# Optimization experiments

Measured on AMD Instinct MI355X. Metric: run time of the kernel, lower is better.

Reference implementation:

```python
import jax, jax.numpy as jnp
import numpy as np

B, T, D, H, FF = 4, 2048, 1024, 16, 4096
HD = D // H
EPS = 1e-5


def setup_inputs() -> dict:
    key = jax.random.key(0)
    ks = jax.random.split(key, 10)
    s = lambda k, shape, fan: jax.random.normal(k, shape, jnp.float32) * (1.0 / np.sqrt(fan))
    return {
        "x": jax.random.normal(ks[0], (B, T, D), jnp.float32),
        "ln1_g": jnp.ones((D,), jnp.float32),
        "ln1_b": jnp.zeros((D,), jnp.float32),
        "qkv_w": s(ks[1], (D, 3 * D), D),
        "qkv_b": jnp.zeros((3 * D,), jnp.float32),
        "proj_w": s(ks[2], (D, D), D),
        "proj_b": jnp.zeros((D,), jnp.float32),
        "ln2_g": jnp.ones((D,), jnp.float32),
        "ln2_b": jnp.zeros((D,), jnp.float32),
        "ff1_w": s(ks[3], (D, FF), D),
        "ff1_b": jnp.zeros((FF,), jnp.float32),
        "ff2_w": s(ks[4], (FF, D), FF),
        "ff2_b": jnp.zeros((D,), jnp.float32),
    }


def _layernorm(x, g, b):
    mu = jnp.mean(x, axis=-1, keepdims=True)
    var = jnp.mean(jnp.square(x - mu), axis=-1, keepdims=True)
    return (x - mu) * jax.lax.rsqrt(var + EPS) * g + b


def reference(x, ln1_g, ln1_b, qkv_w, qkv_b, proj_w, proj_b,
              ln2_g, ln2_b, ff1_w, ff1_b, ff2_w, ff2_b):
    # --- attention sublayer ---
    h = _layernorm(x, ln1_g, ln1_b)
    qkv = h @ qkv_w + qkv_b                      # [B,T,3D]
    q, k, v = jnp.split(qkv, 3, axis=-1)
    q = q.reshape(B, T, H, HD).transpose(0, 2, 1, 3)  # [B,H,T,hd]
    k = k.reshape(B, T, H, HD).transpose(0, 2, 1, 3)
    v = v.reshape(B, T, H, HD).transpose(0, 2, 1, 3)
    att = jnp.einsum('bhqd,bhkd->bhqk', q, k) / np.sqrt(HD)
    causal = jnp.tril(jnp.ones((T, T), bool))
    att = jnp.where(causal, att, jnp.finfo(att.dtype).min)
    att = jax.nn.softmax(att, axis=-1)
    out = jnp.einsum('bhqk,bhkd->bhqd', att, v)  # [B,H,T,hd]
    out = out.transpose(0, 2, 1, 3).reshape(B, T, D)
    x = x + out @ proj_w + proj_b
    # --- MLP sublayer ---
    h = _layernorm(x, ln2_g, ln2_b)
    h = jax.nn.gelu(h @ ff1_w + ff1_b, approximate=True)
    x = x + h @ ff2_w + ff2_b
    return x
```

## Files before the change

### kernel.cpp

```cpp
#include <hip/hip_runtime.h>

typedef __attribute__((ext_vector_type(4))) float f32x4;
typedef __attribute__((ext_vector_type(8))) short s16x8;
typedef __attribute__((ext_vector_type(4))) unsigned short u16x4;

#define DEV __device__ __forceinline__

DEV unsigned short f2bf(float f) {
  unsigned int u = __float_as_uint(f);
  return (unsigned short)((u + 0x7FFFu + ((u >> 16) & 1u)) >> 16);
}

DEV void gload_lds16(const void* g, void* l) {
  __builtin_amdgcn_global_load_lds(
      (const __attribute__((address_space(1))) unsigned int*)g,
      (__attribute__((address_space(3))) unsigned int*)l, 16, 0, 0);
}

__global__ __launch_bounds__(256) void ln_kernel(
    const float* __restrict__ x, const float* __restrict__ gam,
    const float* __restrict__ bet, unsigned short* __restrict__ o)
{
  const int row = blockIdx.x;
  const int tid = threadIdx.x;
  f32x4 v = *(const f32x4*)(x + (size_t)row * 1024 + tid * 4);
  float s = v[0] + v[1] + v[2] + v[3];
  float s2 = v[0]*v[0] + v[1]*v[1] + v[2]*v[2] + v[3]*v[3];
  #pragma unroll
  for (int m = 1; m < 64; m <<= 1) { s += __shfl_xor(s, m); s2 += __shfl_xor(s2, m); }
  __shared__ float ps[4], ps2[4];
  const int wid = tid >> 6, lane = tid & 63;
  if (lane == 0) { ps[wid] = s; ps2[wid] = s2; }
  __syncthreads();
  s = ps[0] + ps[1] + ps[2] + ps[3];
  s2 = ps2[0] + ps2[1] + ps2[2] + ps2[3];
  const float mu = s * (1.0f / 1024.0f);
  const float rstd = rsqrtf(s2 * (1.0f / 1024.0f) - mu * mu + 1e-5f);
  f32x4 g4 = *(const f32x4*)(gam + tid * 4);
  f32x4 b4 = *(const f32x4*)(bet + tid * 4);
  u16x4 ov;
  #pragma unroll
  for (int j = 0; j < 4; j++) ov[j] = f2bf((v[j] - mu) * rstd * g4[j] + b4[j]);
  *(u16x4*)(o + (size_t)row * 1024 + tid * 4) = ov;
}

__global__ __launch_bounds__(256) void transpose_kernel(
    const float* __restrict__ W, unsigned short* __restrict__ WT, int K, int N)
{
  __shared__ float tile[64][65];
  const int n0 = blockIdx.x * 64, k0 = blockIdx.y * 64;
  const int c = threadIdx.x & 63, r0 = threadIdx.x >> 6;
  #pragma unroll
  for (int r = r0; r < 64; r += 4)
    tile[r][c] = W[(size_t)(k0 + r) * N + n0 + c];
  __syncthreads();
  #pragma unroll
  for (int r = r0; r < 64; r += 4)
    WT[(size_t)(n0 + r) * K + k0 + c] = f2bf(tile[c][r]);
}

template <int MODE>
__global__ __launch_bounds__(256) void gemm_kernel(
    const unsigned short* __restrict__ A, const unsigned short* __restrict__ WT,
    const float* __restrict__ bias, const float* resid, void* outp,
    int M, int N, int K)
{
  __shared__ unsigned short As[128 * 32];
  __shared__ unsigned short Bs[128 * 32];
  const int tid = threadIdx.x;
  const int lane = tid & 63;
  const int wid = tid >> 6;
  const int l15 = lane & 15, l4 = lane >> 4;
  const int tiles_n = N >> 7;
  const int cpx = gridDim.x >> 3;
  const int id = (blockIdx.x & 7) * cpx + (blockIdx.x >> 3);
  const int bm = id / tiles_n, bn = id % tiles_n;
  const int wr = wid >> 1, wc = wid & 1;

  f32x4 acc[4][4] = {};

  for (int kt = 0; kt < K; kt += 32) {
    #pragma unroll
    for (int s = 0; s < 2; ++s) {
      const int c = s * 256 + tid;
      const int rowi = c >> 2, colb = (c & 3) * 8;
      unsigned short* lbase_a = As + (size_t)(c & ~63) * 8;
      unsigned short* lbase_b = Bs + (size_t)(c & ~63) * 8;
      gload_lds16(A  + (size_t)(bm * 128 + rowi) * K + kt + colb, lbase_a);
      gload_lds16(WT + (size_t)(bn * 128 + rowi) * K + kt + colb, lbase_b);
    }
    __syncthreads();
    s16x8 af[4], bq[4];
    #pragma unroll
    for (int i = 0; i < 4; i++)
      af[i] = *(const s16x8*)&As[(wr * 64 + i * 16 + l15) * 32 + l4 * 8];
    #pragma unroll
    for (int j = 0; j < 4; j++)
      bq[j] = *(const s16x8*)&Bs[(wc * 64 + j * 16 + l15) * 32 + l4 * 8];
    #pragma unroll
    for (int i = 0; i < 4; i++)
      #pragma unroll
      for (int j = 0; j < 4; j++)
        acc[i][j] = __builtin_amdgcn_mfma_f32_16x16x32_bf16(af[i], bq[j], acc[i][j], 0, 0, 0);
    __syncthreads();
  }

  #pragma unroll
  for (int i = 0; i < 4; i++) {
    #pragma unroll
    for (int j = 0; j < 4; j++) {
      const int col = bn * 128 + wc * 64 + j * 16 + l15;
      const float bv = bias[col];
      #pragma unroll
      for (int r = 0; r < 4; r++) {
        const int row = bm * 128 + wr * 64 + i * 16 + l4 * 4 + r;
        const size_t off = (size_t)row * N + col;
        float v = acc[i][j][r] + bv;
        if (MODE == 1) {
          ((float*)outp)[off] = v + resid[off];
        } else if (MODE == 2) {
          const float t = __expf(1.5957691216f * (v + 0.044715f * v * v * v));
          ((unsigned short*)outp)[off] = f2bf(v - v / (t + 1.0f));
        } else {
          ((unsigned short*)outp)[off] = f2bf(v);
        }
      }
    }
  }
}


struct AttnState {
  f32x4 o[4];
  float m, l;
};

DEV void attn_tile(const s16x8* qf, const unsigned short* Ks,
                   const unsigned short* Vt, unsigned short* Pw,
                   AttnState& st, int kv0, int qg, int l15, int l4, bool need_mask)
{
  f32x4 sa[4];
  #pragma unroll
  for (int cb = 0; cb < 4; cb++) sa[cb] = (f32x4){0.f, 0.f, 0.f, 0.f};
  __builtin_amdgcn_s_setprio(1);
  #pragma unroll
  for (int ks = 0; ks < 2; ++ks) {
    #pragma unroll
    for (int cb = 0; cb < 4; cb++) {
      const int kvr = cb * 16 + l15;
      s16x8 bk = *(const s16x8*)&Ks[kvr * 64 + ((ks * 32 + l4 * 8) ^ ((kvr & 7) << 3))];
      sa[cb] = __builtin_amdgcn_mfma_f32_16x16x32_bf16(bk, qf[ks], sa[cb], 0, 0, 0);
    }
  }
  __builtin_amdgcn_s_setprio(0);
  float mx = -3.0e38f;
  const int thr = qg - kv0 - l4 * 4;
  #pragma unroll
  for (int cb = 0; cb < 4; cb++)
    #pragma unroll
    for (int r = 0; r < 4; r++) {
      float sv = sa[cb][r] * 0.125f;
      if (need_mask && (cb * 16 + r > thr)) sv = -3.0e38f;
      sa[cb][r] = sv;
      mx = fmaxf(mx, sv);
    }
  mx = fmaxf(mx, __shfl_xor(mx, 16));
  mx = fmaxf(mx, __shfl_xor(mx, 32));
  const float mnew = fmaxf(st.m, mx);
  const float alpha = __expf(st.m - mnew);
  st.m = mnew;
  float rsum = 0.f;
  #pragma unroll
  for (int cb = 0; cb < 4; cb++) {
    u16x4 pw;
    #pragma unroll
    for (int r = 0; r < 4; r++) {
      const float p = __expf(sa[cb][r] - mnew);
      rsum += p;
      pw[r] = f2bf(p);
    }
    *(u16x4*)&Pw[l15 * 64 + ((cb * 16 + l4 * 4) ^ ((l15 & 7) << 3))] = pw;
  }
  rsum += __shfl_xor(rsum, 16);
  rsum += __shfl_xor(rsum, 32);
  st.l = st.l * alpha + rsum;
  #pragma unroll
  for (int r = 0; r < 4; r++) {
    const float ar = __shfl(alpha, l4 * 4 + r);
    #pragma unroll
    for (int cb = 0; cb < 4; cb++) st.o[cb][r] *= ar;
  }
  asm volatile("s_waitcnt lgkmcnt(0)" ::: "memory");
  __builtin_amdgcn_s_setprio(1);
  #pragma unroll
  for (int ks = 0; ks < 2; ++ks) {
    s16x8 pa = *(const s16x8*)&Pw[l15 * 64 + ((ks * 32 + l4 * 8) ^ ((l15 & 7) << 3))];
    #pragma unroll
    for (int cb = 0; cb < 4; cb++) {
      const int d = cb * 16 + l15;
      s16x8 vf = *(const s16x8*)&Vt[d * 64 + ((ks * 32 + l4 * 8) ^ (((d >> 2) & 7) << 3))];
      st.o[cb] = __builtin_amdgcn_mfma_f32_16x16x32_bf16(pa, vf, st.o[cb], 0, 0, 0);
    }
  }
  __builtin_amdgcn_s_setprio(0);
}

DEV void attn_write(unsigned short* orow, const AttnState& st, int l15, int l4) {
  const float invl = 1.0f / st.l;
  #pragma unroll
  for (int r = 0; r < 4; r++) {
    const float ir = __shfl(invl, l4 * 4 + r);
    #pragma unroll
    for (int cb = 0; cb < 4; cb++)
      orow[(l4 * 4 + r) * 1024 + cb * 16 + l15] = f2bf(st.o[cb][r] * ir);
  }
}

__global__ __launch_bounds__(256) void attn_kernel(
    const unsigned short* __restrict__ qkv, unsigned short* __restrict__ outb)
{
  __shared__ unsigned short Ks[64 * 64];
  __shared__ unsigned short Vt[64 * 64];
  __shared__ unsigned short Ps[2][4][16 * 64];
  const int pid = blockIdx.x;
  const int qA = pid, qB = 31 - pid;
  const int bh = blockIdx.y;
  const int b = bh >> 4, h = bh & 15;
  const int tid = threadIdx.x, lane = tid & 63, wid = tid >> 6;
  const int l15 = lane & 15, l4 = lane >> 4;
  const size_t base = (size_t)b * 2048 * 3072 + (size_t)h * 64;
  const unsigned short* Qb = qkv + base;
  const unsigned short* Kb = qkv + base + 1024;
  const unsigned short* Vb = qkv + base + 2048;

  s16x8 qfA[2], qfB[2];
  {
    const unsigned short* qr = Qb + (size_t)(qA * 64 + wid * 16 + l15) * 3072 + l4 * 8;
    qfA[0] = *(const s16x8*)qr;
    qfA[1] = *(const s16x8*)(qr + 32);
    qr = Qb + (size_t)(qB * 64 + wid * 16 + l15) * 3072 + l4 * 8;
    qfB[0] = *(const s16x8*)qr;
    qfB[1] = *(const s16x8*)(qr + 32);
  }
  AttnState sA, sB;
  #pragma unroll
  for (int cb = 0; cb < 4; cb++) {
    sA.o[cb] = (f32x4){0.f, 0.f, 0.f, 0.f};
    sB.o[cb] = (f32x4){0.f, 0.f, 0.f, 0.f};
  }
  sA.m = -1e30f; sA.l = 0.f; sB.m = -1e30f; sB.l = 0.f;
  const int qgA = qA * 64 + wid * 16 + l15;
  const int qgB = qB * 64 + wid * 16 + l15;

  for (int kvb = 0; kvb <= qB; ++kvb) {
    const int kv0 = kvb * 64;
    __syncthreads();
    #pragma unroll
    for (int s = 0; s < 2; ++s) {
      const int c = s * 256 + tid;
      const int kv = c >> 3;
      const int dsrc = ((c & 7) * 8) ^ ((kv & 7) << 3);
      gload_lds16(Kb + (size_t)(kv0 + kv) * 3072 + dsrc,
                  Ks + (size_t)(c & ~63) * 8);
    }
    #pragma unroll
    for (int it = 0; it < 4; ++it) {
      const int cc = tid + 256 * it;
      const int vkv = cc >> 4;
      const int vd = (cc & 15) * 4;
      u16x4 vv = *(const u16x4*)(Vb + (size_t)(kv0 + vkv) * 3072 + vd);
      #pragma unroll
      for (int j = 0; j < 4; j++) {
        const int d = vd + j;
        Vt[d * 64 + (vkv ^ (((d >> 2) & 7) << 3))] = vv[j];
      }
    }
    __syncthreads();

    if (kvb <= qA)
      attn_tile(qfA, Ks, Vt, Ps[0][wid], sA, kv0, qgA, l15, l4,
                kv0 + 63 > qA * 64 + wid * 16);
    attn_tile(qfB, Ks, Vt, Ps[1][wid], sB, kv0, qgB, l15, l4,
              kv0 + 63 > qB * 64 + wid * 16);
  }
  attn_write(outb + ((size_t)b * 2048 + qA * 64 + wid * 16) * 1024 + h * 64, sA, l15, l4);
  attn_write(outb + ((size_t)b * 2048 + qB * 64 + wid * 16) * 1024 + h * 64, sB, l15, l4);
}

extern "C" void kernel_launch(void* const* d_in, const int* in_sizes, int n_in,
                              void* d_out, int out_size, void* d_ws, size_t ws_size,
                              hipStream_t stream) {
  const float* x      = (const float*)d_in[0];
  const float* ln1_g  = (const float*)d_in[1];
  const float* ln1_b  = (const float*)d_in[2];
  const float* qkv_w  = (const float*)d_in[3];
  const float* qkv_b  = (const float*)d_in[4];
  const float* proj_w = (const float*)d_in[5];
  const float* proj_b = (const float*)d_in[6];
  const float* ln2_g  = (const float*)d_in[7];
  const float* ln2_b  = (const float*)d_in[8];
  const float* ff1_w  = (const float*)d_in[9];
  const float* ff1_b  = (const float*)d_in[10];
  const float* ff2_w  = (const float*)d_in[11];
  const float* ff2_b  = (const float*)d_in[12];
  float* out = (float*)d_out;

  char* ws = (char*)d_ws;
  size_t off = 0;
  unsigned short* wbuf   = (unsigned short*)(ws + off); off += (size_t)4096 * 1024 * 2;
  unsigned short* hbuf   = (unsigned short*)(ws + off); off += (size_t)8192 * 1024 * 2;
  unsigned short* qkvbuf = (unsigned short*)(ws + off); off += (size_t)8192 * 3072 * 2;
  unsigned short* gbuf   = (unsigned short*)(ws + off);

  ln_kernel<<<8192, 256, 0, stream>>>(x, ln1_g, ln1_b, hbuf);
  transpose_kernel<<<dim3(3072 / 64, 1024 / 64), 256, 0, stream>>>(qkv_w, wbuf, 1024, 3072);
  gemm_kernel<0><<<dim3(64 * 24), 256, 0, stream>>>(hbuf, wbuf, qkv_b, nullptr, qkvbuf,
                                                    8192, 3072, 1024);
  attn_kernel<<<dim3(16, 64), 256, 0, stream>>>(qkvbuf, hbuf);
  transpose_kernel<<<dim3(1024 / 64, 1024 / 64), 256, 0, stream>>>(proj_w, wbuf, 1024, 1024);
  gemm_kernel<1><<<dim3(64 * 8), 256, 0, stream>>>(hbuf, wbuf, proj_b, x, out,
                                                   8192, 1024, 1024);
  ln_kernel<<<8192, 256, 0, stream>>>(out, ln2_g, ln2_b, hbuf);
  transpose_kernel<<<dim3(4096 / 64, 1024 / 64), 256, 0, stream>>>(ff1_w, wbuf, 1024, 4096);
  gemm_kernel<2><<<dim3(64 * 32), 256, 0, stream>>>(hbuf, wbuf, ff1_b, nullptr, gbuf,
                                                    8192, 4096, 1024);
  transpose_kernel<<<dim3(1024 / 64, 4096 / 64), 256, 0, stream>>>(ff2_w, wbuf, 4096, 1024);
  gemm_kernel<1><<<dim3(64 * 8), 256, 0, stream>>>(gbuf, wbuf, ff2_b, out, out,
                                                   8192, 1024, 4096);
}
```

Measured before the change: 534.2 us.

## Add 256x256-tile 8-wave GEMM with 4-stage LDS pipeline for QKV and FF1

```diff
diff --git a/kernel.cpp b/kernel.cpp
--- a/kernel.cpp
+++ b/kernel.cpp
@@ -129,6 +129,112 @@
   }
 }
 
+template <int MODE>
+__global__ __launch_bounds__(512) void gemm8_kernel(
+    const unsigned short* __restrict__ A, const unsigned short* __restrict__ WT,
+    const float* __restrict__ bias, const float* resid, void* outp,
+    int M, int N, int K)
+{
+  __shared__ unsigned short lds[4 * 16384];
+  const int tid = threadIdx.x;
+  const int lane = tid & 63, wid = tid >> 6;
+  const int l15 = lane & 15, l4 = lane >> 4;
+  const int wm = wid >> 2, wn = wid & 3;
+  const int tiles_n = N >> 8;
+  const int cpx = gridDim.x >> 3;
+  const int id = (blockIdx.x & 7) * cpx + (blockIdx.x >> 3);
+  const int bm = id / tiles_n, bn = id % tiles_n;
+  const int NT = K >> 5;
+
+  const int srow = tid >> 2;
+  const int scol = (tid & 3) * 8;
+  const unsigned short* Abase = A  + (size_t)(bm * 256 + srow) * K + scol;
+  const unsigned short* Bbase = WT + (size_t)(bn * 256 + srow) * K + scol;
+  const size_t jstride = (size_t)128 * K;
+  const int dstoff = wid * 512;
+
+  f32x4 acc[8][4] = {};
+
+  const int aoff = (wm * 128 + l15) * 32 + l4 * 8;
+  const int boff = (wn * 64 + l15) * 32 + l4 * 8;
+
+#define STAGE_A(t_) { unsigned short* s_ = lds + ((t_) & 3) * 16384; \
+    gload_lds16(Abase + (size_t)(t_) * 32,           s_ + dstoff); \
+    gload_lds16(Abase + jstride + (size_t)(t_) * 32, s_ + 4096 + dstoff); }
+#define STAGE_B(t_) { unsigned short* s_ = lds + ((t_) & 3) * 16384 + 8192; \
+    gload_lds16(Bbase + (size_t)(t_) * 32,           s_ + dstoff); \
+    gload_lds16(Bbase + jstride + (size_t)(t_) * 32, s_ + 4096 + dstoff); }
+
+  STAGE_A(0); STAGE_B(0);
+  STAGE_A(1); STAGE_B(1);
+  STAGE_A(2); STAGE_B(2);
+  asm volatile("s_waitcnt vmcnt(8)" ::: "memory");
+  __builtin_amdgcn_s_barrier();
+
+  for (int t = 0; t < NT; ++t) {
+    const unsigned short* sa = lds + (t & 3) * 16384;
+    const unsigned short* sb = sa + 8192;
+    s16x8 af[4], bf[4];
+    #pragma unroll
+    for (int mf = 0; mf < 4; mf++) af[mf] = *(const s16x8*)&sa[aoff + mf * 512];
+    #pragma unroll
+    for (int nf = 0; nf < 4; nf++) bf[nf] = *(const s16x8*)&sb[boff + nf * 512];
+    if (t + 3 < NT) STAGE_A(t + 3);
+    __builtin_amdgcn_s_barrier();
+    asm volatile("s_waitcnt lgkmcnt(0)" ::: "memory");
+    __builtin_amdgcn_sched_barrier(0);
+    __builtin_amdgcn_s_setprio(1);
+    #pragma unroll
+    for (int mf = 0; mf < 4; mf++)
+      #pragma unroll
+      for (int nf = 0; nf < 4; nf++)
+        acc[mf][nf] = __builtin_amdgcn_mfma_f32_16x16x32_bf16(af[mf], bf[nf], acc[mf][nf], 0, 0, 0);
+    __builtin_amdgcn_s_setprio(0);
+    __builtin_amdgcn_s_barrier();
+    #pragma unroll
+    for (int mf = 0; mf < 4; mf++) af[mf] = *(const s16x8*)&sa[aoff + (4 + mf) * 512];
+    if (t + 3 < NT) STAGE_B(t + 3);
+    __builtin_amdgcn_s_barrier();
+    asm volatile("s_waitcnt lgkmcnt(0)" ::: "memory");
+    __builtin_amdgcn_sched_barrier(0);
+    __builtin_amdgcn_s_setprio(1);
+    #pragma unroll
+    for (int mf = 0; mf < 4; mf++)
+      #pragma unroll
+      for (int nf = 0; nf < 4; nf++)
+        acc[4 + mf][nf] = __builtin_amdgcn_mfma_f32_16x16x32_bf16(af[mf], bf[nf], acc[4 + mf][nf], 0, 0, 0);
+    __builtin_amdgcn_s_setprio(0);
+    if (t + 3 < NT)      { asm volatile("s_waitcnt vmcnt(8)" ::: "memory"); }
+    else if (t + 2 < NT) { asm volatile("s_waitcnt vmcnt(4)" ::: "memory"); }
+    else if (t + 1 < NT) { asm volatile("s_waitcnt vmcnt(0)" ::: "memory"); }
+    __builtin_amdgcn_s_barrier();
+  }
+#undef STAGE_A
+#undef STAGE_B
+
+  #pragma unroll
+  for (int nf = 0; nf < 4; nf++) {
+    const int col = bn * 256 + wn * 64 + nf * 16 + l15;
+    const float bv = bias[col];
+    #pragma unroll
+    for (int mf = 0; mf < 8; mf++) {
+      #pragma unroll
+      for (int r = 0; r < 4; r++) {
+        const int row = bm * 256 + wm * 128 + mf * 16 + l4 * 4 + r;
+        const size_t off = (size_t)row * N + col;
+        float v = acc[mf][nf][r] + bv;
+        if (MODE == 1) {
+          ((float*)outp)[off] = v + resid[off];
+        } else if (MODE == 2) {
+          const float tt = __expf(1.5957691216f * (v + 0.044715f * v * v * v));
+          ((unsigned short*)outp)[off] = f2bf(v - v / (tt + 1.0f));
+        } else {
+          ((unsigned short*)outp)[off] = f2bf(v);
+        }
+      }
+    }
+  }
+}
 
 struct AttnState {
   f32x4 o[4];
@@ -314,16 +420,16 @@
 
   ln_kernel<<<8192, 256, 0, stream>>>(x, ln1_g, ln1_b, hbuf);
   transpose_kernel<<<dim3(3072 / 64, 1024 / 64), 256, 0, stream>>>(qkv_w, wbuf, 1024, 3072);
-  gemm_kernel<0><<<dim3(64 * 24), 256, 0, stream>>>(hbuf, wbuf, qkv_b, nullptr, qkvbuf,
-                                                    8192, 3072, 1024);
+  gemm8_kernel<0><<<dim3(32 * 12), 512, 0, stream>>>(hbuf, wbuf, qkv_b, nullptr, qkvbuf,
+                                                     8192, 3072, 1024);
   attn_kernel<<<dim3(16, 64), 256, 0, stream>>>(qkvbuf, hbuf);
   transpose_kernel<<<dim3(1024 / 64, 1024 / 64), 256, 0, stream>>>(proj_w, wbuf, 1024, 1024);
   gemm_kernel<1><<<dim3(64 * 8), 256, 0, stream>>>(hbuf, wbuf, proj_b, x, out,
                                                    8192, 1024, 1024);
   ln_kernel<<<8192, 256, 0, stream>>>(out, ln2_g, ln2_b, hbuf);
   transpose_kernel<<<dim3(4096 / 64, 1024 / 64), 256, 0, stream>>>(ff1_w, wbuf, 1024, 4096);
-  gemm_kernel<2><<<dim3(64 * 32), 256, 0, stream>>>(hbuf, wbuf, ff1_b, nullptr, gbuf,
-                                                    8192, 4096, 1024);
+  gemm8_kernel<2><<<dim3(32 * 16), 512, 0, stream>>>(hbuf, wbuf, ff1_b, nullptr, gbuf,
+                                                     8192, 4096, 1024);
   transpose_kernel<<<dim3(1024 / 64, 4096 / 64), 256, 0, stream>>>(ff2_w, wbuf, 4096, 1024);
   gemm_kernel<1><<<dim3(64 * 8), 256, 0, stream>>>(gbuf, wbuf, ff2_b, out, out,
                                                    8192, 1024, 4096);
```

Result: faster. 515.4 us (-3.5%).

## Rewrite GEMM as 8-wave 128x256 tile kernel with triple-buffered swizzled LDS

Applied to the files above, without the earlier changes.

```diff
diff --git a/kernel.cpp b/kernel.cpp
--- a/kernel.cpp
+++ b/kernel.cpp
@@ -60,67 +60,117 @@
 }
 
 template <int MODE>
-__global__ __launch_bounds__(256) void gemm_kernel(
+__global__ __launch_bounds__(512) void gemm8_kernel(
     const unsigned short* __restrict__ A, const unsigned short* __restrict__ WT,
     const float* __restrict__ bias, const float* resid, void* outp,
     int M, int N, int K)
 {
-  __shared__ unsigned short As[128 * 32];
-  __shared__ unsigned short Bs[128 * 32];
+  __shared__ unsigned short lds[3 * 24576];
   const int tid = threadIdx.x;
-  const int lane = tid & 63;
-  const int wid = tid >> 6;
+  const int lane = tid & 63, wid = tid >> 6;
   const int l15 = lane & 15, l4 = lane >> 4;
-  const int tiles_n = N >> 7;
+  const int wm = wid >> 2, wn = wid & 3;
+  const int tiles_n = N >> 8;
   const int cpx = gridDim.x >> 3;
   const int id = (blockIdx.x & 7) * cpx + (blockIdx.x >> 3);
   const int bm = id / tiles_n, bn = id % tiles_n;
-  const int wr = wid >> 1, wc = wid & 1;
+  const int NT = K >> 6;
+
+  const int srow = tid >> 3;
+  const int scol = ((tid & 7) ^ (srow & 7)) * 8;
+  const unsigned short* Asrc = A  + (size_t)(bm * 128 + srow) * K + scol;
+  const unsigned short* Bsrc = WT + (size_t)(bn * 256 + srow) * K + scol;
+  const size_t j64 = (size_t)64 * K;
+  const int dwave = wid * 1024;
+
+#define STAGE(t_, ss_) do { \
+    char* base_ = (char*)lds + (ss_) * 49152 + dwave; \
+    const unsigned short* sA_ = Asrc + (size_t)(t_) * 64; \
+    const unsigned short* sB_ = Bsrc + (size_t)(t_) * 64; \
+    gload_lds16(sA_,            base_); \
+    gload_lds16(sA_ + j64,      base_ + 8192); \
+    gload_lds16(sB_,            base_ + 16384); \
+    gload_lds16(sB_ + j64,      base_ + 16384 + 8192); \
+    gload_lds16(sB_ + 2 * j64,  base_ + 16384 + 16384); \
+    gload_lds16(sB_ + 3 * j64,  base_ + 16384 + 24576); \
+  } while (0)
 
   f32x4 acc[4][4] = {};
 
-  for (int kt = 0; kt < K; kt += 32) {
-    #pragma unroll
-    for (int s = 0; s < 2; ++s) {
-      const int c = s * 256 + tid;
-      const int rowi = c >> 2, colb = (c & 3) * 8;
-      unsigned short* lbase_a = As + (size_t)(c & ~63) * 8;
-      unsigned short* lbase_b = Bs + (size_t)(c & ~63) * 8;
-      gload_lds16(A  + (size_t)(bm * 128 + rowi) * K + kt + colb, lbase_a);
-      gload_lds16(WT + (size_t)(bn * 128 + rowi) * K + kt + colb, lbase_b);
-    }
-    __syncthreads();
-    s16x8 af[4], bq[4];
-    #pragma unroll
-    for (int i = 0; i < 4; i++)
-      af[i] = *(const s16x8*)&As[(wr * 64 + i * 16 + l15) * 32 + l4 * 8];
-    #pragma unroll
-    for (int j = 0; j < 4; j++)
-      bq[j] = *(const s16x8*)&Bs[(wc * 64 + j * 16 + l15) * 32 + l4 * 8];
-    #pragma unroll
-    for (int i = 0; i < 4; i++)
+  const int arow0 = wm * 64 + l15;
+  const int brow0 = wn * 64 + l15;
+  const int cswz = l15 & 7;
+
+  STAGE(0, 0);
+  STAGE(1, 1);
+  asm volatile("s_waitcnt vmcnt(6)" ::: "memory");
+  __builtin_amdgcn_s_barrier();
+
+  int cs = 0, ss = 2;
+  for (int t = 0; t < NT; ++t) {
+    const unsigned short* sa = lds + cs * 24576;
+    const unsigned short* sb = sa + 8192;
+    s16x8 bf[4][2];
+    #pragma unroll
+    for (int p = 0; p < 2; ++p) {
+      s16x8 af[2][2];
       #pragma unroll
-      for (int j = 0; j < 4; j++)
-        acc[i][j] = __builtin_amdgcn_mfma_f32_16x16x32_bf16(af[i], bq[j], acc[i][j], 0, 0, 0);
-    __syncthreads();
-  }
-
-  #pragma unroll
-  for (int i = 0; i < 4; i++) {
-    #pragma unroll
-    for (int j = 0; j < 4; j++) {
-      const int col = bn * 128 + wc * 64 + j * 16 + l15;
-      const float bv = bias[col];
+      for (int mi = 0; mi < 2; ++mi)
+        #pragma unroll
+        for (int ks = 0; ks < 2; ++ks) {
+          const int row = arow0 + (p * 2 + mi) * 16;
+          af[mi][ks] = *(const s16x8*)&sa[row * 64 + (((ks * 4 + l4) ^ cswz) * 8)];
+        }
+      if (p == 0) {
+        #pragma unroll
+        for (int nf = 0; nf < 4; ++nf)
+          #pragma unroll
+          for (int ks = 0; ks < 2; ++ks) {
+            const int row = brow0 + nf * 16;
+            bf[nf][ks] = *(const s16x8*)&sb[row * 64 + (((ks * 4 + l4) ^ cswz) * 8)];
+          }
+        if (t + 2 < NT) STAGE(t + 2, ss);
+      }
+      __builtin_amdgcn_s_barrier();
+      asm volatile("s_waitcnt lgkmcnt(0)" ::: "memory");
+      __builtin_amdgcn_sched_barrier(0);
+      __builtin_amdgcn_s_setprio(1);
+      #pragma unroll
+      for (int mi = 0; mi < 2; ++mi)
+        #pragma unroll
+        for (int nf = 0; nf < 4; ++nf)
+          #pragma unroll
+          for (int ks = 0; ks < 2; ++ks)
+            acc[p * 2 + mi][nf] = __builtin_amdgcn_mfma_f32_16x16x32_bf16(
+                af[mi][ks], bf[nf][ks], acc[p * 2 + mi][nf], 0, 0, 0);
+      __builtin_amdgcn_s_setprio(0);
+      if (p == 1) {
+        if (t + 2 < NT)      { asm volatile("s_waitcnt vmcnt(6)" ::: "memory"); }
+        else if (t + 1 < NT) { asm volatile("s_waitcnt vmcnt(0)" ::: "memory"); }
+      }
+      __builtin_amdgcn_s_barrier();
+    }
+    cs = (cs == 2) ? 0 : cs + 1;
+    ss = (ss == 2) ? 0 : ss + 1;
+  }
+#undef STAGE
+
+  #pragma unroll
+  for (int nf = 0; nf < 4; nf++) {
+    const int col = bn * 256 + wn * 64 + nf * 16 + l15;
+    const float bv = bias[col];
+    #pragma unroll
+    for (int mf = 0; mf < 4; mf++) {
       #pragma unroll
       for (int r = 0; r < 4; r++) {
-        const int row = bm * 128 + wr * 64 + i * 16 + l4 * 4 + r;
+        const int row = bm * 128 + wm * 64 + mf * 16 + l4 * 4 + r;
         const size_t off = (size_t)row * N + col;
-        float v = acc[i][j][r] + bv;
+        float v = acc[mf][nf][r] + bv;
         if (MODE == 1) {
           ((float*)outp)[off] = v + resid[off];
         } else if (MODE == 2) {
-          const float t = __expf(1.5957691216f * (v + 0.044715f * v * v * v));
-          ((unsigned short*)outp)[off] = f2bf(v - v / (t + 1.0f));
+          const float tt = __expf(1.5957691216f * (v + 0.044715f * v * v * v));
+          ((unsigned short*)outp)[off] = f2bf(v - v / (tt + 1.0f));
         } else {
           ((unsigned short*)outp)[off] = f2bf(v);
         }
@@ -128,7 +178,6 @@
     }
   }
 }
-
 
 struct AttnState {
   f32x4 o[4];
@@ -314,17 +363,17 @@
 
   ln_kernel<<<8192, 256, 0, stream>>>(x, ln1_g, ln1_b, hbuf);
   transpose_kernel<<<dim3(3072 / 64, 1024 / 64), 256, 0, stream>>>(qkv_w, wbuf, 1024, 3072);
-  gemm_kernel<0><<<dim3(64 * 24), 256, 0, stream>>>(hbuf, wbuf, qkv_b, nullptr, qkvbuf,
-                                                    8192, 3072, 1024);
+  gemm8_kernel<0><<<dim3(64 * 12), 512, 0, stream>>>(hbuf, wbuf, qkv_b, nullptr, qkvbuf,
+                                                     8192, 3072, 1024);
   attn_kernel<<<dim3(16, 64), 256, 0, stream>>>(qkvbuf, hbuf);
   transpose_kernel<<<dim3(1024 / 64, 1024 / 64), 256, 0, stream>>>(proj_w, wbuf, 1024, 1024);
-  gemm_kernel<1><<<dim3(64 * 8), 256, 0, stream>>>(hbuf, wbuf, proj_b, x, out,
-                                                   8192, 1024, 1024);
+  gemm8_kernel<1><<<dim3(64 * 4), 512, 0, stream>>>(hbuf, wbuf, proj_b, x, out,
+                                                    8192, 1024, 1024);
   ln_kernel<<<8192, 256, 0, stream>>>(out, ln2_g, ln2_b, hbuf);
   transpose_kernel<<<dim3(4096 / 64, 1024 / 64), 256, 0, stream>>>(ff1_w, wbuf, 1024, 4096);
-  gemm_kernel<2><<<dim3(64 * 32), 256, 0, stream>>>(hbuf, wbuf, ff1_b, nullptr, gbuf,
-                                                    8192, 4096, 1024);
+  gemm8_kernel<2><<<dim3(64 * 16), 512, 0, stream>>>(hbuf, wbuf, ff1_b, nullptr, gbuf,
+                                                     8192, 4096, 1024);
   transpose_kernel<<<dim3(1024 / 64, 4096 / 64), 256, 0, stream>>>(ff2_w, wbuf, 4096, 1024);
-  gemm_kernel<1><<<dim3(64 * 8), 256, 0, stream>>>(gbuf, wbuf, ff2_b, out, out,
-                                                   8192, 1024, 4096);
-}
+  gemm8_kernel<1><<<dim3(64 * 4), 512, 0, stream>>>(gbuf, wbuf, ff2_b, out, out,
+                                                    8192, 1024, 4096);
+}
```

After: 471.2 us. 11.8% less time.
